# Optimization experiments

Hardware: AMD Instinct MI355X
Metric: run time of the kernel (lower is better)

## Reference

```python
import jax, jax.numpy as jnp
import numpy as np

N, E, IN, K, F, D = 50000, 800000, 256, 4, 64, 2


def setup_inputs() -> dict:
    key = jax.random.key(0)
    ks = jax.random.split(key, 10)
    # CSR rowptr: 0 .. E, nondecreasing, endpoints pinned
    inner = jnp.sort(jax.random.randint(ks[0], (N - 1,), 0, E + 1))
    rowptr = jnp.concatenate([jnp.zeros(1, jnp.int64), inner.astype(jnp.int64), jnp.full(1, E, jnp.int64)])
    colind = jax.random.randint(ks[1], (E,), 0, N).astype(jnp.int64)
    # CSC mirrors (used only by the fused kernel's backward; inert in forward math)
    inner_c = jnp.sort(jax.random.randint(ks[2], (N - 1,), 0, E + 1))
    colptr = jnp.concatenate([jnp.zeros(1, jnp.int64), inner_c.astype(jnp.int64), jnp.full(1, E, jnp.int64)])
    rowind = jax.random.randint(ks[3], (E,), 0, N).astype(jnp.int64)
    permute = jnp.arange(E, dtype=jnp.int64)
    feat = jax.random.normal(ks[4], (N, IN), dtype=jnp.float32)
    pseudo = jax.random.uniform(ks[5], (E, D), dtype=jnp.float32)
    # params: fc weight [K*F, IN] (xavier-normal style scale), mu ~ N(0, 0.1), inv_sigma = 1, bias = 0
    gain = float(np.sqrt(2.0))
    std = gain * float(np.sqrt(2.0 / (IN + K * F)))
    W_fc = jax.random.normal(ks[6], (K * F, IN), dtype=jnp.float32) * std
    mu = jax.random.normal(ks[7], (K, D), dtype=jnp.float32) * 0.1
    inv_sigma = jnp.ones((K, D), dtype=jnp.float32)
    bias = jnp.zeros((F,), dtype=jnp.float32)
    return {"rowptr": rowptr, "colind": colind, "colptr": colptr, "rowind": rowind,
            "permute": permute, "feat": feat, "pseudo": pseudo,
            "W_fc": W_fc, "mu": mu, "inv_sigma": inv_sigma, "bias": bias}


def reference(rowptr, colind, colptr, rowind, permute, feat, pseudo, W_fc, mu, inv_sigma, bias):
    n = feat.shape[0]
    e = colind.shape[0]
    k, d = mu.shape
    f = W_fc.shape[0] // k
    # dense projection: [N, K, F]
    node_feat = (feat @ W_fc.T).reshape(n, k, f)
    # per-edge Gaussian mixture weights: [E, K]
    diff = pseudo[:, None, :] - mu[None, :, :]              # [E, K, D]
    gaussian = jnp.exp(jnp.sum(-0.5 * diff * diff * (inv_sigma[None, :, :] ** 2), axis=-1))
    # multi-head SpMM: gather source feats, weight per kernel, sum kernels (sum commutes
    # with the segment reduction, so fold the head-sum into the edge message): [E, F]
    msg = jnp.einsum('ek,ekf->ef', gaussian, node_feat[colind])
    # destination node of each CSR edge
    dst = jnp.searchsorted(rowptr, jnp.arange(e), side='right') - 1
    rst = jax.ops.segment_sum(msg, dst, num_segments=n)      # [N, F]
    return rst + bias
```

## Files before the change

### kernel.cpp

```cpp
#include <hip/hip_runtime.h>


typedef _Float16 f16;
typedef __attribute__((ext_vector_type(4))) _Float16 f16x4;
typedef __attribute__((ext_vector_type(8))) _Float16 f16x8;
typedef __attribute__((ext_vector_type(4))) float f32x4;

__device__ inline f16x4 cvt4h(float4 v) {
    f16x4 h;
    h.x = (f16)v.x; h.y = (f16)v.y; h.z = (f16)v.z; h.w = (f16)v.w;
    return h;
}

__device__ inline int dot4_i8(int a, int b) {
#if __has_builtin(__builtin_amdgcn_sdot4)
    return __builtin_amdgcn_sdot4(a, b, 0, false);
#else
    return (int)(char)(a)       * (int)(char)(b)
         + (int)(char)(a >> 8)  * (int)(char)(b >> 8)
         + (int)(char)(a >> 16) * (int)(char)(b >> 16)
         + (int)(char)(a >> 24) * (int)(char)(b >> 24);
#endif
}

__global__ __launch_bounds__(256) void convert_W(
    const float* __restrict__ W, f16* __restrict__ Wp)
{
    const int gid = blockIdx.x * 256 + threadIdx.x;
    const int jp = gid >> 6, k4 = gid & 63;
    const int wrow = ((jp & 3) << 6) | (jp >> 2);
    reinterpret_cast<f16x4*>(Wp)[jp * 64 + k4] =
        cvt4h(reinterpret_cast<const float4*>(W)[wrow * 64 + k4]);
}

#define ASTRIDE 264
#define AS_BYTES (64 * ASTRIDE * 2)

__global__ __launch_bounds__(256) void gemm_fused(
    const float* __restrict__ feat,
    const f16* __restrict__ Wp,
    char* __restrict__ nfq,
    float* __restrict__ sc,
    int M)
{
    __shared__ char smem[AS_BYTES + 256 * 32 * 2];
    f16* As = (f16*)smem;
    f16* Bs = (f16*)(smem + AS_BYTES);
    char* qt = smem + AS_BYTES;
    const int t    = threadIdx.x;
    const int lane = t & 63;
    const int wave = t >> 6;
    const int bm   = blockIdx.x * 64;
    const int l16  = lane & 15;
    const int quad = lane >> 4;
    const int wn   = wave * 64;

    size_t bsrc[4];
#pragma unroll
    for (int j = 0; j < 4; ++j)
        bsrc[j] = (size_t)(wave * 64 + j * 16 + (lane >> 2)) * 256 + (lane & 3) * 8;

    typedef __attribute__((address_space(3))) void lds_t;
    typedef const __attribute__((address_space(1))) void gm_t;

#pragma unroll
    for (int j = 0; j < 4; ++j)
        __builtin_amdgcn_global_load_lds((gm_t*)(Wp + bsrc[j]),
            (lds_t*)(Bs + (wave * 4 + j) * 512), 16, 0, 0);

#pragma unroll
    for (int it = 0; it < 8; ++it) {
        const int flat = it * 2048 + t * 8;
        const int row  = flat >> 8;
        const int koff = flat & 255;
        const float* src = feat + (size_t)min(bm + row, M - 1) * 256 + koff;
        const float4 a0 = *reinterpret_cast<const float4*>(src);
        const float4 a1 = *reinterpret_cast<const float4*>(src + 4);
        *reinterpret_cast<f16x4*>(&As[row * ASTRIDE + koff])     = cvt4h(a0);
        *reinterpret_cast<f16x4*>(&As[row * ASTRIDE + koff + 4]) = cvt4h(a1);
    }

    f32x4 acc[4][4];
#pragma unroll
    for (int mi = 0; mi < 4; ++mi)
#pragma unroll
        for (int ni = 0; ni < 4; ++ni)
            acc[mi][ni] = (f32x4){0.f, 0.f, 0.f, 0.f};

    for (int ki = 0; ki < 8; ++ki) {
        __syncthreads();

        f16x8 af[4], bfr[4];
#pragma unroll
        for (int mi = 0; mi < 4; ++mi)
            af[mi] = *reinterpret_cast<const f16x8*>(
                &As[(mi * 16 + l16) * ASTRIDE + ki * 32 + quad * 8]);
#pragma unroll
        for (int ni = 0; ni < 4; ++ni)
            bfr[ni] = *reinterpret_cast<const f16x8*>(
                &Bs[(wn + ni * 16 + l16) * 32 + quad * 8]);

        __syncthreads();
        if (ki < 7) {
            const int k0 = (ki + 1) * 32;
#pragma unroll
            for (int j = 0; j < 4; ++j)
                __builtin_amdgcn_global_load_lds((gm_t*)(Wp + bsrc[j] + k0),
                    (lds_t*)(Bs + (wave * 4 + j) * 512), 16, 0, 0);
        }
#pragma unroll
        for (int mi = 0; mi < 4; ++mi)
#pragma unroll
            for (int ni = 0; ni < 4; ++ni)
                acc[mi][ni] = __builtin_amdgcn_mfma_f32_16x16x32_f16(
                    af[mi], bfr[ni], acc[mi][ni], 0, 0, 0);
    }

#pragma unroll
    for (int mi = 0; mi < 4; ++mi) {
#pragma unroll
        for (int r = 0; r < 4; ++r) {
            float am = 0.f;
#pragma unroll
            for (int ni = 0; ni < 4; ++ni)
                am = fmaxf(am, fabsf(acc[mi][ni][r]));
            am = fmaxf(am, __shfl_xor(am, 1));
            am = fmaxf(am, __shfl_xor(am, 2));
            am = fmaxf(am, __shfl_xor(am, 4));
            am = fmaxf(am, __shfl_xor(am, 8));
            const float sinv = am > 0.f ? 127.f / am : 0.f;
            const int rl = mi * 16 + quad * 4 + r;
#pragma unroll
            for (int ni = 0; ni < 4; ++ni)
                qt[rl * 256 + wn + ni * 16 + l16] =
                    (char)(int)__builtin_rintf(acc[mi][ni][r] * sinv);
            if (l16 == 0) {
                const int row = bm + rl;
                if (row < M) sc[row * 4 + wave] = am * (1.f / 16129.f);
            }
        }
    }
    __syncthreads();

    {
        const int rl  = t >> 2;
        const int co  = (t & 3) * 64;
        const int row = bm + rl;
        if (row < M) {
            const int4* s4 = reinterpret_cast<const int4*>(qt + rl * 256 + co);
            int4* d4 = reinterpret_cast<int4*>(nfq + (size_t)row * 256 + co);
#pragma unroll
            for (int j = 0; j < 4; ++j) d4[j] = s4[j];
        }
    }
}

__global__ __launch_bounds__(128) void edge_aggregate(
    const int* __restrict__ rowptr,
    const int* __restrict__ colind,
    const float* __restrict__ pseudo,
    const char* __restrict__ nfq,
    const float* __restrict__ sc,
    const float* __restrict__ mu,
    const float* __restrict__ inv_sigma,
    const float* __restrict__ bias,
    float* __restrict__ out,
    int N)
{
    __shared__ int gpack[2][16];
    __shared__ int cbuf[2][16];
    const int wave = threadIdx.x >> 6;
    const int lane = threadIdx.x & 63;
    const int node = blockIdx.x * 2 + wave;
    if (node >= N) return;

    const int kk = lane >> 4;
    const int ii = lane & 15;
    const float mx = mu[2 * kk], my = mu[2 * kk + 1];
    const float sa = inv_sigma[2 * kk], sb = inv_sigma[2 * kk + 1];
    const float sx = sa * sa, sy = sb * sb;

    const int e0 = rowptr[node];
    const int e1 = rowptr[node + 1];
    int* gp = gpack[wave];
    int* cw = cbuf[wave];

    float a4[4] = {0.f, 0.f, 0.f, 0.f};
    for (int ec = e0; ec < e1; ec += 16) {
        const int cnt = min(16, e1 - ec);
        {
            const bool v = ii < cnt;
            const int e = v ? (ec + ii) : e0;
            const float2 p = *reinterpret_cast<const float2*>(pseudo + 2 * (size_t)e);
            const float dx = p.x - mx, dy = p.y - my;
            const float g = v ? __expf(-0.5f * (dx * dx * sx + dy * dy * sy)) : 0.f;
            ((char*)&gp[ii])[kk] = (char)(int)(g * 127.f + 0.5f);
            if (kk == 0) cw[ii] = v ? colind[e] : 0;
        }
        __builtin_amdgcn_wave_barrier();
        __threadfence_block();
        const int cnt4 = (cnt + 3) & ~3;
        for (int i2 = 0; i2 < cnt4; i2 += 4) {
#pragma unroll
            for (int j = 0; j < 4; ++j) {
                const int c = cw[i2 + j];
                const int q = *reinterpret_cast<const int*>(
                    nfq + ((size_t)c << 8) + (lane << 2));
                const float s = sc[c * 4 + (lane >> 4)];
                const int d = dot4_i8(q, gp[i2 + j]);
                a4[j] += s * (float)d;
            }
        }
        __builtin_amdgcn_wave_barrier();
        __threadfence_block();
    }
    out[((size_t)node << 6) + lane] =
        (a4[0] + a4[1]) + (a4[2] + a4[3]) + bias[lane];
}

extern "C" void kernel_launch(void* const* d_in, const int* in_sizes, int n_in,
                              void* d_out, int out_size, void* d_ws, size_t ws_size,
                              hipStream_t stream)
{
    const int*   rowptr    = (const int*)d_in[0];
    const int*   colind    = (const int*)d_in[1];
    const float* feat      = (const float*)d_in[5];
    const float* pseudo    = (const float*)d_in[6];
    const float* W_fc      = (const float*)d_in[7];
    const float* mu        = (const float*)d_in[8];
    const float* inv_sigma = (const float*)d_in[9];
    const float* bias      = (const float*)d_in[10];
    float* out = (float*)d_out;

    const int N = in_sizes[0] - 1;
    char*  nfq = (char*)d_ws;
    float* sc  = (float*)(nfq + (size_t)N * 256);
    f16*   Wp  = (f16*)d_out;

    hipLaunchKernelGGL(convert_W, dim3(64), dim3(256), 0, stream, W_fc, Wp);

    hipLaunchKernelGGL(gemm_fused, dim3((N + 63) / 64), dim3(256), 0, stream,
                       feat, Wp, nfq, sc, N);

    hipLaunchKernelGGL(edge_aggregate, dim3((N + 1) / 2), dim3(128), 0, stream,
                       rowptr, colind, pseudo, nfq, sc, mu, inv_sigma, bias, out, N);
}
```

Before: 182.6 us.

## Precompute packed Gaussian edge weights and batch gathers via wave shuffles

Per-edge Gaussian weights are now computed once for all edges in a prep kernel, which also converts W, and stored as packed int8. The aggregation kernel reads those weights directly, so it no longer computes exp or reads pseudo per chunk. It also drops the LDS staging and wave barriers in favour of register shuffles, and issues all 16 neighbour gathers per chunk before using any of them, to raise memory-level parallelism. The cost is an extra pass over the edges and a 4-byte-per-edge workspace array, plus higher register use from holding 16 loaded values at once.

```diff
diff --git a/kernel.cpp b/kernel.cpp
--- a/kernel.cpp
+++ b/kernel.cpp
@@ -23,14 +23,37 @@
 #endif
 }
 
-__global__ __launch_bounds__(256) void convert_W(
-    const float* __restrict__ W, f16* __restrict__ Wp)
+__global__ __launch_bounds__(256) void prep(
+    const float* __restrict__ W, const float* __restrict__ pseudo,
+    const float* __restrict__ mu, const float* __restrict__ inv_sigma,
+    f16* __restrict__ Wp, int* __restrict__ gq, int E)
 {
     const int gid = blockIdx.x * 256 + threadIdx.x;
-    const int jp = gid >> 6, k4 = gid & 63;
-    const int wrow = ((jp & 3) << 6) | (jp >> 2);
-    reinterpret_cast<f16x4*>(Wp)[jp * 64 + k4] =
-        cvt4h(reinterpret_cast<const float4*>(W)[wrow * 64 + k4]);
+    if (gid < 16384) {
+        const int jp = gid >> 6, k4 = gid & 63;
+        const int wrow = ((jp & 3) << 6) | (jp >> 2);
+        reinterpret_cast<f16x4*>(Wp)[jp * 64 + k4] =
+            cvt4h(reinterpret_cast<const float4*>(W)[wrow * 64 + k4]);
+    }
+    float mx[4], my[4], sx[4], sy[4];
+#pragma unroll
+    for (int k = 0; k < 4; ++k) {
+        mx[k] = mu[2 * k];
+        my[k] = mu[2 * k + 1];
+        const float a = inv_sigma[2 * k], b = inv_sigma[2 * k + 1];
+        sx[k] = a * a; sy[k] = b * b;
+    }
+    for (int e = gid; e < E; e += gridDim.x * 256) {
+        const float2 p = reinterpret_cast<const float2*>(pseudo)[e];
+        int pack = 0;
+#pragma unroll
+        for (int k = 0; k < 4; ++k) {
+            const float dx = p.x - mx[k], dy = p.y - my[k];
+            const float g = __expf(-0.5f * (dx * dx * sx[k] + dy * dy * sy[k]));
+            pack |= ((int)(g * 127.f + 0.5f) & 0xff) << (8 * k);
+        }
+        gq[e] = pack;
+    }
 }
 
 #define ASTRIDE 264
@@ -158,61 +181,47 @@
 __global__ __launch_bounds__(128) void edge_aggregate(
     const int* __restrict__ rowptr,
     const int* __restrict__ colind,
-    const float* __restrict__ pseudo,
+    const int* __restrict__ gq,
     const char* __restrict__ nfq,
     const float* __restrict__ sc,
-    const float* __restrict__ mu,
-    const float* __restrict__ inv_sigma,
     const float* __restrict__ bias,
     float* __restrict__ out,
     int N)
 {
-    __shared__ int gpack[2][16];
-    __shared__ int cbuf[2][16];
-    const int wave = threadIdx.x >> 6;
     const int lane = threadIdx.x & 63;
-    const int node = blockIdx.x * 2 + wave;
+    const int node = (blockIdx.x * blockDim.x + threadIdx.x) >> 6;
     if (node >= N) return;
 
     const int kk = lane >> 4;
     const int ii = lane & 15;
-    const float mx = mu[2 * kk], my = mu[2 * kk + 1];
-    const float sa = inv_sigma[2 * kk], sb = inv_sigma[2 * kk + 1];
-    const float sx = sa * sa, sy = sb * sb;
 
     const int e0 = rowptr[node];
     const int e1 = rowptr[node + 1];
-    int* gp = gpack[wave];
-    int* cw = cbuf[wave];
 
     float a4[4] = {0.f, 0.f, 0.f, 0.f};
     for (int ec = e0; ec < e1; ec += 16) {
         const int cnt = min(16, e1 - ec);
-        {
-            const bool v = ii < cnt;
-            const int e = v ? (ec + ii) : e0;
-            const float2 p = *reinterpret_cast<const float2*>(pseudo + 2 * (size_t)e);
-            const float dx = p.x - mx, dy = p.y - my;
-            const float g = v ? __expf(-0.5f * (dx * dx * sx + dy * dy * sy)) : 0.f;
-            ((char*)&gp[ii])[kk] = (char)(int)(g * 127.f + 0.5f);
-            if (kk == 0) cw[ii] = v ? colind[e] : 0;
-        }
-        __builtin_amdgcn_wave_barrier();
-        __threadfence_block();
-        const int cnt4 = (cnt + 3) & ~3;
-        for (int i2 = 0; i2 < cnt4; i2 += 4) {
-#pragma unroll
-            for (int j = 0; j < 4; ++j) {
-                const int c = cw[i2 + j];
-                const int q = *reinterpret_cast<const int*>(
-                    nfq + ((size_t)c << 8) + (lane << 2));
-                const float s = sc[c * 4 + (lane >> 4)];
-                const int d = dot4_i8(q, gp[i2 + j]);
-                a4[j] += s * (float)d;
-            }
-        }
-        __builtin_amdgcn_wave_barrier();
-        __threadfence_block();
+        const bool v = ii < cnt;
+        const int idx = v ? (ec + ii) : e0;
+        const int c  = colind[idx];
+        int g4 = gq[idx];
+        if (!v) g4 = 0;
+        const float s = sc[c * 4 + kk];
+
+        int cj[16];
+#pragma unroll
+        for (int j = 0; j < 16; ++j) cj[j] = __shfl(c, j);
+        int qj[16];
+#pragma unroll
+        for (int j = 0; j < 16; ++j)
+            qj[j] = *reinterpret_cast<const int*>(
+                nfq + ((size_t)cj[j] << 8) + (lane << 2));
+#pragma unroll
+        for (int j = 0; j < 16; ++j) {
+            const int   gj = __shfl(g4, j);
+            const float sj = __shfl(s, (kk << 4) | j);
+            a4[j & 3] += sj * (float)dot4_i8(qj[j], gj);
+        }
     }
     out[((size_t)node << 6) + lane] =
         (a4[0] + a4[1]) + (a4[2] + a4[3]) + bias[lane];
@@ -233,15 +242,18 @@
     float* out = (float*)d_out;
 
     const int N = in_sizes[0] - 1;
+    const int E = in_sizes[1];
     char*  nfq = (char*)d_ws;
     float* sc  = (float*)(nfq + (size_t)N * 256);
+    int*   gq  = (int*)(sc + (size_t)N * 4);
     f16*   Wp  = (f16*)d_out;
 
-    hipLaunchKernelGGL(convert_W, dim3(64), dim3(256), 0, stream, W_fc, Wp);
+    hipLaunchKernelGGL(prep, dim3(1024), dim3(256), 0, stream,
+                       W_fc, pseudo, mu, inv_sigma, Wp, gq, E);
 
     hipLaunchKernelGGL(gemm_fused, dim3((N + 63) / 64), dim3(256), 0, stream,
                        feat, Wp, nfq, sc, N);
 
-    hipLaunchKernelGGL(edge_aggregate, dim3((N + 1) / 2), dim3(128), 0, stream,
-                       rowptr, colind, pseudo, nfq, sc, mu, inv_sigma, bias, out, N);
-}
+    hipLaunchKernelGGL(edge_aggregate, dim3((N * 64 + 127) / 128), dim3(128), 0,
+                       stream, rowptr, colind, gq, nfq, sc, bias, out, N);
+}
```

New measurement: 186.3 us. 1.02x slower.
